# Optimization experiments

Hardware: AMD Instinct MI355X
Metric: run time of the kernel (lower is better)

Reference implementation:

```python
import jax, jax.numpy as jnp
import numpy as np

BATCH = 2048
INPUT_SIZE = 2048
OUTPUT_SIZE = 2048
N_INPUTS = 6            # fan-in per LUT node
K = 1 << N_INPUTS       # 64 table entries per node


def setup_inputs() -> dict:
    key = jax.random.key(0)
    k1, k2, k3 = jax.random.split(key, 3)
    x = jax.random.uniform(k1, (BATCH, INPUT_SIZE), dtype=jnp.float32)
    table = jax.random.normal(k2, (OUTPUT_SIZE, K), dtype=jnp.float32)
    mapping = jax.random.randint(k3, (OUTPUT_SIZE, N_INPUTS), 0, INPUT_SIZE, dtype=jnp.int64)
    return {"x": x, "table": table, "mapping": mapping}


def reference(x, table, mapping):
    # x: (B, I) in [0,1]; table: (O, 2^n) raw logits; mapping: (O, n) int indices
    O, n = mapping.shape
    Kv = 1 << n
    # per-node input gather -> (B, O, n)
    xg = x[:, mapping]
    # binary codes of the 2^n LUT vertices: bits[k, i] = i-th bit of k
    bits = ((jnp.arange(Kv)[:, None] >> jnp.arange(n)[None, :]) & 1).astype(x.dtype)  # (K, n)
    # vertex probabilities prod_i (x_i if bit else 1-x_i), built by a tiny fixed loop over n
    probs = jnp.ones((x.shape[0], O, Kv), dtype=x.dtype)
    for i in range(n):
        xi = xg[:, :, i][:, :, None]                      # (B, O, 1)
        bi = bits[:, i][None, None, :]                    # (1, 1, K)
        probs = probs * (xi * bi + (1.0 - xi) * (1.0 - bi))
    # differentiable LUT lookup: expected table value under vertex distribution
    out = jnp.einsum('bok,ok->bo', probs, jax.nn.sigmoid(table))  # (B, O)
    return out
```

## Files before the change

### kernel.cpp

```cpp
#include <hip/hip_runtime.h>
#include <math.h>

#define B_TOTAL 2048
#define I_TOTAL 2048
#define O_TOTAL 2048
#define KW 64
#define NIN 6
#define BLOCK 256
#define TILE_B 16
#define CH 2
#define NCHUNK (TILE_B / CH)
#define BBLOCKS (B_TOTAL / TILE_B)
#define OBLOCKS (O_TOTAL / BLOCK)

__global__ __launch_bounds__(BLOCK) void prep_kernel(
    const float* __restrict__ table,
    const unsigned int* __restrict__ map_raw,
    float* __restrict__ wT,
    int* __restrict__ m32T)
{
    const int t = threadIdx.x;

    if (blockIdx.x < 32) {
        __shared__ float sm[64][65];
        const int o0 = blockIdx.x * 64;
        #pragma unroll
        for (int rep = 0; rep < 16; ++rep) {
            int idx = rep * 256 + t;
            int ol = idx >> 6, k = idx & 63;
            float v = table[(o0 + ol) * KW + k];
            sm[ol][k] = 1.0f / (1.0f + __expf(-v));
        }
        __syncthreads();
        #pragma unroll
        for (int rep = 0; rep < 16; ++rep) {
            int idx = rep * 256 + t;
            int k = idx >> 6, ol = idx & 63;
            float s = sm[ol][k];
            float v = (k >= 32) ? (s - sm[ol][k - 32]) : s;
            wT[k * O_TOTAL + o0 + ol] = v;
        }
    }

    const int gid = blockIdx.x * BLOCK + t;
    if (gid < O_TOTAL * NIN) {
        bool is64 = ((map_raw[1] | map_raw[3] | map_raw[5] | map_raw[7]) == 0u);
        int val = is64 ? (int)map_raw[2 * gid] : (int)map_raw[gid];
        int oo = gid / NIN, ii = gid - oo * NIN;
        m32T[ii * O_TOTAL + oo] = val;
    }
}

__device__ __forceinline__ void async_cp16(float* lds, const float* g)
{
    __builtin_amdgcn_global_load_lds(
        (const __attribute__((address_space(1))) void*)g,
        (__attribute__((address_space(3))) void*)lds,
        16, 0, 0);
}

__global__ __launch_bounds__(BLOCK, 3) void lut_main(
    const float* __restrict__ x,
    const float* __restrict__ wT,
    const int*   __restrict__ m32T,
    float*       __restrict__ out)
{
    __shared__ float xs[2 * CH * I_TOTAL];

    const int o    = blockIdx.y * BLOCK + threadIdx.x;
    const int b0   = blockIdx.x * TILE_B;
    const int wave = threadIdx.x >> 6;
    const int lane = threadIdx.x & 63;

    float ww[KW];
    #pragma unroll
    for (int k = 0; k < KW; ++k) ww[k] = wT[k * O_TOTAL + o];

    int m[NIN];
    #pragma unroll
    for (int i = 0; i < NIN; ++i) m[i] = m32T[i * O_TOTAL + o];

    {
        const float* src = x + (size_t)b0 * I_TOTAL;
        #pragma unroll
        for (int ti = 0; ti < 4; ++ti) {
            int off = (wave * 4 + ti) * 256;
            async_cp16(&xs[off], src + off + lane * 4);
        }
    }
    __syncthreads();

    #pragma unroll 2
    for (int c = 0; c < NCHUNK; ++c) {
        const int buf = c & 1;

        if (c + 1 < NCHUNK) {
            const float* src = x + (size_t)(b0 + (c + 1) * CH) * I_TOTAL;
            float* dst = &xs[(buf ^ 1) * CH * I_TOTAL];
            #pragma unroll
            for (int ti = 0; ti < 4; ++ti) {
                int off = (wave * 4 + ti) * 256;
                async_cp16(dst + off, src + off + lane * 4);
            }
        }

        #pragma unroll
        for (int cr = 0; cr < CH; ++cr) {
            const int rowc = (buf * CH + cr) * I_TOTAL;
            float xv[NIN];
            #pragma unroll
            for (int i = 0; i < NIN; ++i) xv[i] = xs[rowc + m[i]];

            float tt[32];
            #pragma unroll
            for (int j = 0; j < 32; ++j) tt[j] = fmaf(xv[5], ww[j + 32], ww[j]);
            #pragma unroll
            for (int j = 0; j < 16; ++j) tt[j] = fmaf(xv[4], tt[j + 16] - tt[j], tt[j]);
            #pragma unroll
            for (int j = 0; j < 8;  ++j) tt[j] = fmaf(xv[3], tt[j + 8]  - tt[j], tt[j]);
            #pragma unroll
            for (int j = 0; j < 4;  ++j) tt[j] = fmaf(xv[2], tt[j + 4]  - tt[j], tt[j]);
            #pragma unroll
            for (int j = 0; j < 2;  ++j) tt[j] = fmaf(xv[1], tt[j + 2]  - tt[j], tt[j]);
            float res = fmaf(xv[0], tt[1] - tt[0], tt[0]);

            out[(size_t)(b0 + c * CH + cr) * O_TOTAL + o] = res;
        }

        __syncthreads();
    }
}

extern "C" void kernel_launch(void* const* d_in, const int* in_sizes, int n_in,
                              void* d_out, int out_size, void* d_ws, size_t ws_size,
                              hipStream_t stream)
{
    const float*        x       = (const float*)d_in[0];
    const float*        table   = (const float*)d_in[1];
    const unsigned int* map_raw = (const unsigned int*)d_in[2];
    float* out  = (float*)d_out;
    float* wT   = (float*)d_ws;
    int*   m32T = (int*)((char*)d_ws + (size_t)O_TOTAL * KW * sizeof(float));

    prep_kernel<<<48, BLOCK, 0, stream>>>(table, map_raw, wT, m32T);

    dim3 grid(BBLOCKS, OBLOCKS);
    lut_main<<<grid, dim3(BLOCK), 0, stream>>>(x, wT, m32T, out);
}
```

Measured before the change: 85.28 us.

## Stage 8-row x tile once and loop over output chunks per block

Each block now loads a tile of 8 full rows of x into LDS once and then loops over four 256-wide output chunks, reloading the table weights and mapping for each chunk. This replaces the double-buffered 2-row pipeline over 16 rows with a single fill and no per-chunk barriers, so x rows are reused across 1024 outputs instead of 256. The cost is that weights are reloaded per chunk, there is no overlap between the x load and compute, and LDS use grows to 64KB per block with occupancy lowered to 2.

Result: no change. 86.86 us (+1.9%).

```diff
diff --git a/kernel.cpp b/kernel.cpp
--- a/kernel.cpp
+++ b/kernel.cpp
@@ -7,11 +7,10 @@
 #define KW 64
 #define NIN 6
 #define BLOCK 256
-#define TILE_B 16
-#define CH 2
-#define NCHUNK (TILE_B / CH)
-#define BBLOCKS (B_TOTAL / TILE_B)
-#define OBLOCKS (O_TOTAL / BLOCK)
+#define TILE_B 8
+#define T_O 1024
+#define OC_N (T_O / BLOCK)
+#define MAIN_BLOCKS ((B_TOTAL / TILE_B) * (O_TOTAL / T_O))
 
 __global__ __launch_bounds__(BLOCK) void prep_kernel(
     const float* __restrict__ table,
@@ -59,57 +58,47 @@
         16, 0, 0);
 }
 
-__global__ __launch_bounds__(BLOCK, 3) void lut_main(
+__global__ __launch_bounds__(BLOCK, 2) void lut_main(
     const float* __restrict__ x,
     const float* __restrict__ wT,
     const int*   __restrict__ m32T,
     float*       __restrict__ out)
 {
-    __shared__ float xs[2 * CH * I_TOTAL];
+    __shared__ float xs[TILE_B * I_TOTAL];
 
-    const int o    = blockIdx.y * BLOCK + threadIdx.x;
-    const int b0   = blockIdx.x * TILE_B;
-    const int wave = threadIdx.x >> 6;
-    const int lane = threadIdx.x & 63;
-
-    float ww[KW];
-    #pragma unroll
-    for (int k = 0; k < KW; ++k) ww[k] = wT[k * O_TOTAL + o];
-
-    int m[NIN];
-    #pragma unroll
-    for (int i = 0; i < NIN; ++i) m[i] = m32T[i * O_TOTAL + o];
+    const int tid   = threadIdx.x;
+    const int btile = blockIdx.x & 255;
+    const int ohalf = blockIdx.x >> 8;
+    const int b0    = btile * TILE_B;
+    const int obase = ohalf * T_O;
 
     {
         const float* src = x + (size_t)b0 * I_TOTAL;
         #pragma unroll
-        for (int ti = 0; ti < 4; ++ti) {
-            int off = (wave * 4 + ti) * 256;
-            async_cp16(&xs[off], src + off + lane * 4);
+        for (int it = 0; it < (TILE_B * I_TOTAL / 4) / BLOCK; ++it) {
+            int f = it * BLOCK + tid;
+            async_cp16(&xs[4 * f], src + 4 * f);
         }
     }
     __syncthreads();
 
-    #pragma unroll 2
-    for (int c = 0; c < NCHUNK; ++c) {
-        const int buf = c & 1;
+    for (int oc = 0; oc < OC_N; ++oc) {
+        const int o = obase + oc * BLOCK + tid;
 
-        if (c + 1 < NCHUNK) {
-            const float* src = x + (size_t)(b0 + (c + 1) * CH) * I_TOTAL;
-            float* dst = &xs[(buf ^ 1) * CH * I_TOTAL];
-            #pragma unroll
-            for (int ti = 0; ti < 4; ++ti) {
-                int off = (wave * 4 + ti) * 256;
-                async_cp16(dst + off, src + off + lane * 4);
-            }
-        }
+        int mm[NIN];
+        #pragma unroll
+        for (int i = 0; i < NIN; ++i) mm[i] = m32T[i * O_TOTAL + o];
+
+        float ww[KW];
+        #pragma unroll
+        for (int k = 0; k < KW; ++k) ww[k] = wT[k * O_TOTAL + o];
 
         #pragma unroll
-        for (int cr = 0; cr < CH; ++cr) {
-            const int rowc = (buf * CH + cr) * I_TOTAL;
+        for (int r = 0; r < TILE_B; ++r) {
+            const float* xr = xs + r * I_TOTAL;
             float xv[NIN];
             #pragma unroll
-            for (int i = 0; i < NIN; ++i) xv[i] = xs[rowc + m[i]];
+            for (int i = 0; i < NIN; ++i) xv[i] = xr[mm[i]];
 
             float tt[32];
             #pragma unroll
@@ -124,10 +113,8 @@
             for (int j = 0; j < 2;  ++j) tt[j] = fmaf(xv[1], tt[j + 2]  - tt[j], tt[j]);
             float res = fmaf(xv[0], tt[1] - tt[0], tt[0]);
 
-            out[(size_t)(b0 + c * CH + cr) * O_TOTAL + o] = res;
+            out[(size_t)(b0 + r) * O_TOTAL + o] = res;
         }
-
-        __syncthreads();
     }
 }
 
@@ -144,6 +131,5 @@
 
     prep_kernel<<<48, BLOCK, 0, stream>>>(table, map_raw, wT, m32T);
 
-    dim3 grid(BBLOCKS, OBLOCKS);
-    lut_main<<<grid, dim3(BLOCK), 0, stream>>>(x, wT, m32T, out);
+    lut_main<<<MAIN_BLOCKS, BLOCK, 0, stream>>>(x, wT, m32T, out);
 }
```

## Interleave x row pairs in prep kernel and use packed FP32 FMA

Applied to the files above, without the earlier changes.

The prep kernel now also writes x with adjacent batch rows interleaved into float2 pairs in workspace. The main kernel then loads both rows' gathered inputs with a single 8-byte LDS read per fan-in index and evaluates the multilinear interpolation with packed two-wide FMAs (v_pk_fma_f32), halving LDS gather instructions and ALU issue. The cost is an extra full pass over x (read plus write of 16 MB) in the prep kernel and higher register pressure from the f32x2 temporaries.

Measured after the change: 132.3 us. +55.1%, slower.

```diff
diff --git a/kernel.cpp b/kernel.cpp
--- a/kernel.cpp
+++ b/kernel.cpp
@@ -8,22 +8,30 @@
 #define NIN 6
 #define BLOCK 256
 #define TILE_B 16
-#define CH 2
-#define NCHUNK (TILE_B / CH)
+#define NPAIR (TILE_B / 2)
 #define BBLOCKS (B_TOTAL / TILE_B)
 #define OBLOCKS (O_TOTAL / BLOCK)
+#define XPREP_BLOCKS (B_TOTAL / 2)
+
+typedef __attribute__((ext_vector_type(2))) float f32x2;
+
+static __device__ __forceinline__ f32x2 sp(float s) { f32x2 v; v.x = s; v.y = s; return v; }
+static __device__ __forceinline__ f32x2 pfma(f32x2 a, f32x2 b, f32x2 c)
+{ return __builtin_elementwise_fma(a, b, c); }
 
 __global__ __launch_bounds__(BLOCK) void prep_kernel(
+    const float* __restrict__ x,
     const float* __restrict__ table,
     const unsigned int* __restrict__ map_raw,
     float* __restrict__ wT,
-    int* __restrict__ m32T)
+    int*   __restrict__ m32T,
+    float* __restrict__ xP)
 {
-    const int t = threadIdx.x;
+    const int t = threadIdx.x, bid = blockIdx.x;
 
-    if (blockIdx.x < 32) {
+    if (bid < 32) {
         __shared__ float sm[64][65];
-        const int o0 = blockIdx.x * 64;
+        const int o0 = bid * 64;
         #pragma unroll
         for (int rep = 0; rep < 16; ++rep) {
             int idx = rep * 256 + t;
@@ -40,9 +48,20 @@
             float v = (k >= 32) ? (s - sm[ol][k - 32]) : s;
             wT[k * O_TOTAL + o0 + ol] = v;
         }
+    } else if (bid >= 48) {
+        const int bp = bid - 48;
+        const float* r0 = x + (size_t)(2 * bp) * I_TOTAL;
+        const float* r1 = r0 + I_TOTAL;
+        f32x2* dst = (f32x2*)(xP + (size_t)bp * 2 * I_TOTAL);
+        #pragma unroll
+        for (int it = 0; it < I_TOTAL / BLOCK; ++it) {
+            int i = it * BLOCK + t;
+            f32x2 v; v.x = r0[i]; v.y = r1[i];
+            dst[i] = v;
+        }
     }
 
-    const int gid = blockIdx.x * BLOCK + t;
+    const int gid = bid * BLOCK + t;
     if (gid < O_TOTAL * NIN) {
         bool is64 = ((map_raw[1] | map_raw[3] | map_raw[5] | map_raw[7]) == 0u);
         int val = is64 ? (int)map_raw[2 * gid] : (int)map_raw[gid];
@@ -60,12 +79,12 @@
 }
 
 __global__ __launch_bounds__(BLOCK, 3) void lut_main(
-    const float* __restrict__ x,
+    const float* __restrict__ xP,
     const float* __restrict__ wT,
     const int*   __restrict__ m32T,
     float*       __restrict__ out)
 {
-    __shared__ float xs[2 * CH * I_TOTAL];
+    __shared__ float xs[2 * 2 * I_TOTAL];
 
     const int o    = blockIdx.y * BLOCK + threadIdx.x;
     const int b0   = blockIdx.x * TILE_B;
@@ -80,23 +99,22 @@
     #pragma unroll
     for (int i = 0; i < NIN; ++i) m[i] = m32T[i * O_TOTAL + o];
 
-    {
-        const float* src = x + (size_t)b0 * I_TOTAL;
-        #pragma unroll
-        for (int ti = 0; ti < 4; ++ti) {
-            int off = (wave * 4 + ti) * 256;
-            async_cp16(&xs[off], src + off + lane * 4);
-        }
+    const float* psrc = xP + (size_t)(b0 >> 1) * 2 * I_TOTAL;
+
+    #pragma unroll
+    for (int ti = 0; ti < 4; ++ti) {
+        int off = (wave * 4 + ti) * 256;
+        async_cp16(&xs[off], psrc + off + lane * 4);
     }
     __syncthreads();
 
     #pragma unroll 2
-    for (int c = 0; c < NCHUNK; ++c) {
+    for (int c = 0; c < NPAIR; ++c) {
         const int buf = c & 1;
 
-        if (c + 1 < NCHUNK) {
-            const float* src = x + (size_t)(b0 + (c + 1) * CH) * I_TOTAL;
-            float* dst = &xs[(buf ^ 1) * CH * I_TOTAL];
+        if (c + 1 < NPAIR) {
+            const float* src = psrc + (size_t)(c + 1) * 2 * I_TOTAL;
+            float* dst = &xs[(buf ^ 1) * 2 * I_TOTAL];
             #pragma unroll
             for (int ti = 0; ti < 4; ++ti) {
                 int off = (wave * 4 + ti) * 256;
@@ -104,28 +122,27 @@
             }
         }
 
+        const int base = buf * 2 * I_TOTAL;
+        f32x2 xv[NIN];
         #pragma unroll
-        for (int cr = 0; cr < CH; ++cr) {
-            const int rowc = (buf * CH + cr) * I_TOTAL;
-            float xv[NIN];
-            #pragma unroll
-            for (int i = 0; i < NIN; ++i) xv[i] = xs[rowc + m[i]];
+        for (int i = 0; i < NIN; ++i)
+            xv[i] = *(const f32x2*)(xs + base + 2 * m[i]);
 
-            float tt[32];
-            #pragma unroll
-            for (int j = 0; j < 32; ++j) tt[j] = fmaf(xv[5], ww[j + 32], ww[j]);
-            #pragma unroll
-            for (int j = 0; j < 16; ++j) tt[j] = fmaf(xv[4], tt[j + 16] - tt[j], tt[j]);
-            #pragma unroll
-            for (int j = 0; j < 8;  ++j) tt[j] = fmaf(xv[3], tt[j + 8]  - tt[j], tt[j]);
-            #pragma unroll
-            for (int j = 0; j < 4;  ++j) tt[j] = fmaf(xv[2], tt[j + 4]  - tt[j], tt[j]);
-            #pragma unroll
-            for (int j = 0; j < 2;  ++j) tt[j] = fmaf(xv[1], tt[j + 2]  - tt[j], tt[j]);
-            float res = fmaf(xv[0], tt[1] - tt[0], tt[0]);
+        f32x2 tt[32];
+        #pragma unroll
+        for (int j = 0; j < 32; ++j) tt[j] = pfma(xv[5], sp(ww[j + 32]), sp(ww[j]));
+        #pragma unroll
+        for (int j = 0; j < 16; ++j) tt[j] = pfma(xv[4], tt[j + 16] - tt[j], tt[j]);
+        #pragma unroll
+        for (int j = 0; j < 8;  ++j) tt[j] = pfma(xv[3], tt[j + 8]  - tt[j], tt[j]);
+        #pragma unroll
+        for (int j = 0; j < 4;  ++j) tt[j] = pfma(xv[2], tt[j + 4]  - tt[j], tt[j]);
+        #pragma unroll
+        for (int j = 0; j < 2;  ++j) tt[j] = pfma(xv[1], tt[j + 2]  - tt[j], tt[j]);
+        f32x2 res = pfma(xv[0], tt[1] - tt[0], tt[0]);
 
-            out[(size_t)(b0 + c * CH + cr) * O_TOTAL + o] = res;
-        }
+        out[(size_t)(b0 + 2 * c)     * O_TOTAL + o] = res.x;
+        out[(size_t)(b0 + 2 * c + 1) * O_TOTAL + o] = res.y;
 
         __syncthreads();
     }
@@ -139,11 +156,14 @@
     const float*        table   = (const float*)d_in[1];
     const unsigned int* map_raw = (const unsigned int*)d_in[2];
     float* out  = (float*)d_out;
+
     float* wT   = (float*)d_ws;
-    int*   m32T = (int*)((char*)d_ws + (size_t)O_TOTAL * KW * sizeof(float));
+    int*   m32T = (int*)((char*)d_ws + (size_t)512 * 1024);
+    float* xP   = (float*)((char*)d_ws + (size_t)1024 * 1024);
 
-    prep_kernel<<<48, BLOCK, 0, stream>>>(table, map_raw, wT, m32T);
+    prep_kernel<<<48 + XPREP_BLOCKS, BLOCK, 0, stream>>>(
+        x, table, map_raw, wT, m32T, xP);
 
     dim3 grid(BBLOCKS, OBLOCKS);
-    lut_main<<<grid, dim3(BLOCK), 0, stream>>>(x, wT, m32T, out);
+    lut_main<<<grid, dim3(BLOCK), 0, stream>>>(xP, wT, m32T, out);
 }
```

## Split each LUT node's 64-entry table across lane pairs to cut registers

Applied to the files above, without the earlier changes.

Each output node is now handled by two adjacent lanes, each holding half of the 64 table weights (32 registers instead of 64). Each lane evaluates a 5-level subtree for both batch rows using values exchanged by lane shuffles, and the final level combines the halves via another shuffle. The prep kernel's differencing is changed to match the new split. Launch bounds are raised from 3 to 5 blocks per SM to exploit the lower register pressure. In exchange, the grid doubles in the output dimension, so x tiles are staged into LDS twice as often, and extra shuffles and duplicated subtree work are added per row.

New measurement: 94.43 us. 10.7% more time.

```diff
diff --git a/kernel.cpp b/kernel.cpp
--- a/kernel.cpp
+++ b/kernel.cpp
@@ -10,8 +10,9 @@
 #define TILE_B 16
 #define CH 2
 #define NCHUNK (TILE_B / CH)
+#define OGROUP (BLOCK / 2)
 #define BBLOCKS (B_TOTAL / TILE_B)
-#define OBLOCKS (O_TOTAL / BLOCK)
+#define OBLOCKS (O_TOTAL / OGROUP)
 
 __global__ __launch_bounds__(BLOCK) void prep_kernel(
     const float* __restrict__ table,
@@ -37,7 +38,7 @@
             int idx = rep * 256 + t;
             int k = idx >> 6, ol = idx & 63;
             float s = sm[ol][k];
-            float v = (k >= 32) ? (s - sm[ol][k - 32]) : s;
+            float v = ((k & 31) >= 16) ? (s - sm[ol][k - 16]) : s;
             wT[k * O_TOTAL + o0 + ol] = v;
         }
     }
@@ -59,7 +60,22 @@
         16, 0, 0);
 }
 
-__global__ __launch_bounds__(BLOCK, 3) void lut_main(
+__device__ __forceinline__ float subtree5(const float* __restrict__ ww,
+                                          const float xv[5])
+{
+    float t[16];
+    #pragma unroll
+    for (int j = 0; j < 16; ++j) t[j] = fmaf(xv[4], ww[j + 16], ww[j]);
+    #pragma unroll
+    for (int j = 0; j < 8;  ++j) t[j] = fmaf(xv[3], t[j + 8] - t[j], t[j]);
+    #pragma unroll
+    for (int j = 0; j < 4;  ++j) t[j] = fmaf(xv[2], t[j + 4] - t[j], t[j]);
+    #pragma unroll
+    for (int j = 0; j < 2;  ++j) t[j] = fmaf(xv[1], t[j + 2] - t[j], t[j]);
+    return fmaf(xv[0], t[1] - t[0], t[0]);
+}
+
+__global__ __launch_bounds__(BLOCK, 5) void lut_main(
     const float* __restrict__ x,
     const float* __restrict__ wT,
     const int*   __restrict__ m32T,
@@ -67,18 +83,12 @@
 {
     __shared__ float xs[2 * CH * I_TOTAL];
 
-    const int o    = blockIdx.y * BLOCK + threadIdx.x;
+    const int tid  = threadIdx.x;
+    const int h    = tid & 1;
+    const int o    = blockIdx.y * OGROUP + (tid >> 1);
     const int b0   = blockIdx.x * TILE_B;
-    const int wave = threadIdx.x >> 6;
-    const int lane = threadIdx.x & 63;
-
-    float ww[KW];
-    #pragma unroll
-    for (int k = 0; k < KW; ++k) ww[k] = wT[k * O_TOTAL + o];
-
-    int m[NIN];
-    #pragma unroll
-    for (int i = 0; i < NIN; ++i) m[i] = m32T[i * O_TOTAL + o];
+    const int wave = tid >> 6;
+    const int lane = tid & 63;
 
     {
         const float* src = x + (size_t)b0 * I_TOTAL;
@@ -88,14 +98,23 @@
             async_cp16(&xs[off], src + off + lane * 4);
         }
     }
+
+    float ww[32];
+    #pragma unroll
+    for (int j = 0; j < 32; ++j) ww[j] = wT[(h * 32 + j) * O_TOTAL + o];
+
+    int m[NIN];
+    #pragma unroll
+    for (int i = 0; i < NIN; ++i) m[i] = m32T[i * O_TOTAL + o];
+
     __syncthreads();
 
     #pragma unroll 2
-    for (int c = 0; c < NCHUNK; ++c) {
-        const int buf = c & 1;
+    for (int cc = 0; cc < NCHUNK; ++cc) {
+        const int buf = cc & 1;
 
-        if (c + 1 < NCHUNK) {
-            const float* src = x + (size_t)(b0 + (c + 1) * CH) * I_TOTAL;
+        if (cc + 1 < NCHUNK) {
+            const float* src = x + (size_t)(b0 + (cc + 1) * CH) * I_TOTAL;
             float* dst = &xs[(buf ^ 1) * CH * I_TOTAL];
             #pragma unroll
             for (int ti = 0; ti < 4; ++ti) {
@@ -104,28 +123,26 @@
             }
         }
 
+        const int rowc0 = (buf * CH) * I_TOTAL;
+        const int myrow = rowc0 + h * I_TOTAL;
+        float g[NIN];
         #pragma unroll
-        for (int cr = 0; cr < CH; ++cr) {
-            const int rowc = (buf * CH + cr) * I_TOTAL;
-            float xv[NIN];
-            #pragma unroll
-            for (int i = 0; i < NIN; ++i) xv[i] = xs[rowc + m[i]];
+        for (int i = 0; i < NIN; ++i) g[i] = xs[myrow + m[i]];
 
-            float tt[32];
-            #pragma unroll
-            for (int j = 0; j < 32; ++j) tt[j] = fmaf(xv[5], ww[j + 32], ww[j]);
-            #pragma unroll
-            for (int j = 0; j < 16; ++j) tt[j] = fmaf(xv[4], tt[j + 16] - tt[j], tt[j]);
-            #pragma unroll
-            for (int j = 0; j < 8;  ++j) tt[j] = fmaf(xv[3], tt[j + 8]  - tt[j], tt[j]);
-            #pragma unroll
-            for (int j = 0; j < 4;  ++j) tt[j] = fmaf(xv[2], tt[j + 4]  - tt[j], tt[j]);
-            #pragma unroll
-            for (int j = 0; j < 2;  ++j) tt[j] = fmaf(xv[1], tt[j + 2]  - tt[j], tt[j]);
-            float res = fmaf(xv[0], tt[1] - tt[0], tt[0]);
+        float xo[5];
+        #pragma unroll
+        for (int i = 0; i < 5; ++i) xo[i] = __shfl_xor(g[i], 1);
 
-            out[(size_t)(b0 + c * CH + cr) * O_TOTAL + o] = res;
-        }
+        float A = subtree5(ww, g);
+        float B = subtree5(ww, xo);
+
+        float Tp = __shfl_xor(B, 1);
+
+        float T0 = h ? Tp : A;
+        float T1 = h ? A  : Tp;
+        float res = fmaf(g[5], T1 - T0, T0);
+
+        out[(size_t)(b0 + cc * CH + h) * O_TOTAL + o] = res;
 
         __syncthreads();
     }
```
